# Optimization experiments

Measured on AMD Instinct MI355X. Metric: run time of the kernel, lower is better.

## Reference

```python
import jax, jax.numpy as jnp
import numpy as np

N_IN, N_OUT, F, H, E, V = 80, 25, 4096, 512, 512, 4096
B = 128
BOS = V - 3  # vocab = sorted words + ['<PAD>', '<BOS>', '<EOS>', '<UNK>']
LEAK = 0.01  # torch leaky_relu default slope


def gru_cell(x, h, wih, whh, bih, bhh):
    # PyTorch GRU gate order: [r, z, n]
    gi = x @ wih.T + bih
    gh = h @ whh.T + bhh
    ir, iz, inn = jnp.split(gi, 3, axis=-1)
    hr, hz, hn = jnp.split(gh, 3, axis=-1)
    r = jax.nn.sigmoid(ir + hr)
    z = jax.nn.sigmoid(iz + hz)
    n = jnp.tanh(inn + r * hn)
    return (1.0 - z) * n + z * h


def run_gru(xs, h0, wih, whh, bih, bhh):
    # xs: [T, B, D] -> outputs [T, B, H], final hidden [B, H]
    def step(h, x):
        h2 = gru_cell(x, h, wih, whh, bih, bhh)
        return h2, h2
    hT, ys = jax.lax.scan(step, h0, xs)
    return ys, hT


def setup_inputs() -> dict:
    key = jax.random.key(0)
    ks = jax.random.split(key, 10)

    def w(k, shape, fan_in):
        return jax.random.normal(k, shape, dtype=jnp.float32) / np.float32(np.sqrt(fan_in))

    return {
        "feats": jax.random.normal(ks[0], (N_IN, B, F), dtype=jnp.float32),
        "fc_w": w(ks[1], (E, F), F),
        "fc_b": jnp.zeros((E,), jnp.float32),
        "enc_wih": w(ks[2], (3 * H, E), E),
        "enc_whh": w(ks[3], (3 * H, H), H),
        "enc_bih": jnp.zeros((3 * H,), jnp.float32),
        "enc_bhh": jnp.zeros((3 * H,), jnp.float32),
        "dec_wih": w(ks[4], (3 * H, 2 * H + E), 2 * H + E),
        "dec_whh": w(ks[5], (3 * H, H), H),
        "dec_bih": jnp.zeros((3 * H,), jnp.float32),
        "dec_bhh": jnp.zeros((3 * H,), jnp.float32),
        "out_w": w(ks[6], (V, H), H),
        "out_b": jnp.zeros((V,), jnp.float32),
        "embed": jax.random.normal(ks[7], (V, E), dtype=jnp.float32) * 0.05,
        "tgt": jax.random.randint(ks[8], (B, N_OUT), 0, V, dtype=jnp.int32),
        "tfr": 0,
    }


def reference(feats, fc_w, fc_b, enc_wih, enc_whh, enc_bih, enc_bhh,
              dec_wih, dec_whh, dec_bih, dec_bhh, out_w, out_b, embed,
              tgt, tfr):
    T_in, Bv, _ = feats.shape
    # fc + leaky_relu (dropout = identity in eval)
    xp = jax.nn.leaky_relu(feats @ fc_w.T + fc_b, LEAK)            # [T_in, B, E]
    e_seq = jnp.concatenate([xp, jnp.zeros((N_OUT, Bv, E), xp.dtype)], axis=0)
    h0 = jnp.zeros((Bv, H), xp.dtype)
    enc_out, _ = run_gru(e_seq, h0, enc_wih, enc_whh, enc_bih, enc_bhh)  # [T_in+N_OUT, B, H]
    encA = jnp.transpose(enc_out[:T_in], (1, 0, 2))                # [B, T_in, H]
    # decoder pass 1 over encoding stage: input = [zeros(H+E) ; enc_out]
    dec1_in = jnp.concatenate(
        [jnp.zeros((T_in, Bv, H + E), xp.dtype), enc_out[:T_in]], axis=-1)
    _, alpha = run_gru(dec1_in, h0, dec_wih, dec_whh, dec_bih, dec_bhh)  # [B, H]

    d0 = jnp.broadcast_to(embed[BOS], (Bv, E))                     # <BOS> embedding
    enc_tail = enc_out[T_in:T_in + N_OUT]                          # [N_OUT, B, H]
    tgt_T = tgt.T                                                  # [N_OUT, B]

    def step(carry, inp):
        h, d = carry
        et_j, t_j = inp
        # dot-product attention over the T_in encoder states (Att_ linear is unused)
        s = jnp.tanh(jnp.einsum('bih,bh->bi', encA, h))            # [B, T_in]
        w = jax.nn.softmax(s, axis=1)
        c = jnp.einsum('bi,bih->bh', w, encA)                      # [B, H]
        x = jnp.concatenate([d, et_j, c], axis=-1)                 # [B, E+2H]
        h2 = gru_cell(x, h, dec_wih, dec_whh, dec_bih, dec_bhh)
        logp = jax.nn.log_softmax(h2 @ out_w.T + out_b, axis=-1)   # [B, V]
        lj = -jnp.mean(jnp.take_along_axis(logp, t_j[:, None], axis=1))
        d_next = embed[jnp.argmax(logp, axis=-1)]                  # greedy feedback (tfr=-1)
        return (h2, d_next), lj

    _, losses = jax.lax.scan(step, (alpha, d0), (enc_tail, tgt_T))
    return jnp.sum(losses) / N_OUT
```

## Files before the change

kernel.cpp:

```cpp
#include <hip/hip_runtime.h>
#include <hip/hip_bf16.h>

#define N_OUT 25
#define BOS   4093

typedef __attribute__((ext_vector_type(8))) short bf16x8;
typedef __attribute__((ext_vector_type(4))) float f32x4;

__device__ inline unsigned short f2bf(float f) {
    unsigned int u = __builtin_bit_cast(unsigned int, f);
    unsigned int r = (u + 0x7fffu + ((u >> 16) & 1u)) >> 16;
    return (unsigned short)r;
}
__device__ inline float bf2f(unsigned short s) {
    return __builtin_bit_cast(float, (unsigned int)s << 16);
}
__device__ inline float sigf(float x) { return 1.f / (1.f + expf(-x)); }

__device__ __forceinline__ unsigned long long ld_u64_coh(const void* p) {
    return __hip_atomic_load((const unsigned long long*)p, __ATOMIC_RELAXED, __HIP_MEMORY_SCOPE_AGENT);
}
__device__ __forceinline__ void st_u64_coh(void* p, unsigned long long v) {
    __hip_atomic_store((unsigned long long*)p, v, __ATOMIC_RELAXED, __HIP_MEMORY_SCOPE_AGENT);
}
__device__ __forceinline__ void st_u32_coh(void* p, unsigned int v) {
    __hip_atomic_store((unsigned int*)p, v, __ATOMIC_RELAXED, __HIP_MEMORY_SCOPE_AGENT);
}
__device__ __forceinline__ unsigned short ld_u16_coh(const unsigned short* p) {
    return __hip_atomic_load(p, __ATOMIC_RELAXED, __HIP_MEMORY_SCOPE_AGENT);
}
__device__ __forceinline__ int ld_i32_coh(const int* p) {
    return __hip_atomic_load(p, __ATOMIC_RELAXED, __HIP_MEMORY_SCOPE_AGENT);
}
__device__ __forceinline__ void st_i32_coh(int* p, int v) {
    __hip_atomic_store(p, v, __ATOMIC_RELAXED, __HIP_MEMORY_SCOPE_AGENT);
}
__device__ inline unsigned long long pack_ff(float a, float b) {
    return ((unsigned long long)__builtin_bit_cast(unsigned int, b) << 32) |
           __builtin_bit_cast(unsigned int, a);
}
__device__ inline unsigned long long pack_if(int a, float b) {
    return ((unsigned long long)__builtin_bit_cast(unsigned int, b) << 32) |
           (unsigned int)a;
}
__device__ __forceinline__ void spin_ge(const int* p, int tgt)
{
    while (ld_i32_coh(p) < tgt) __builtin_amdgcn_s_sleep(1);
}

__device__ __forceinline__ bf16x8 ld_bf8_sc1(const unsigned short* p) {
    bf16x8 r;
    asm volatile("global_load_dwordx4 %0, %1, off sc1" : "=v"(r) : "v"(p));
    return r;
}
#define VM_FENCE do { asm volatile("s_waitcnt vmcnt(0)" ::: "memory"); \
                      __builtin_amdgcn_sched_barrier(0); } while (0)

template<int AFP32, int OUT_BF, int ACT>
__global__ __launch_bounds__(256)
void gemm_mfma(const void* __restrict__ Ap, int lda,
               const unsigned short* __restrict__ W, int ldw,
               const float* __restrict__ bias,
               void* __restrict__ Cp, int ldc, int K)
{
    __shared__ short Abuf[128 * 32];
    __shared__ short Wbuf[128 * 32];
    const int tid  = threadIdx.x;
    const int lane = tid & 63;
    const int wave = tid >> 6;
    const int wr = wave >> 1, wc = wave & 1;
    const int l15 = lane & 15, kg = lane >> 4;
    const int m0 = blockIdx.y * 128, n0 = blockIdx.x * 128;

    const float* Af = (const float*)Ap;
    const unsigned short* Ab = (const unsigned short*)Ap;

    f32x4 acc[4][4];
#pragma unroll
    for (int i = 0; i < 4; ++i)
#pragma unroll
        for (int j = 0; j < 4; ++j) acc[i][j] = f32x4{0.f, 0.f, 0.f, 0.f};

    const bf16x8* Av = (const bf16x8*)Abuf;
    const bf16x8* Wv = (const bf16x8*)Wbuf;

    for (int k0 = 0; k0 < K; k0 += 32) {
#pragma unroll
        for (int cc = 0; cc < 2; ++cc) {
            int c = tid + cc * 256;
            int row = c >> 2, k8 = (c & 3) * 8;
            if (AFP32) {
                const float* src = &Af[(size_t)(m0 + row) * lda + k0 + k8];
                float4 v0 = *reinterpret_cast<const float4*>(src);
                float4 v1 = *reinterpret_cast<const float4*>(src + 4);
                bf16x8 s;
                s[0] = (short)f2bf(v0.x); s[1] = (short)f2bf(v0.y);
                s[2] = (short)f2bf(v0.z); s[3] = (short)f2bf(v0.w);
                s[4] = (short)f2bf(v1.x); s[5] = (short)f2bf(v1.y);
                s[6] = (short)f2bf(v1.z); s[7] = (short)f2bf(v1.w);
                *reinterpret_cast<bf16x8*>(&Abuf[row * 32 + k8]) = s;
            } else {
                *reinterpret_cast<bf16x8*>(&Abuf[row * 32 + k8]) =
                    *reinterpret_cast<const bf16x8*>(&Ab[(size_t)(m0 + row) * lda + k0 + k8]);
            }
            *reinterpret_cast<bf16x8*>(&Wbuf[row * 32 + k8]) =
                *reinterpret_cast<const bf16x8*>(&W[(size_t)(n0 + row) * ldw + k0 + k8]);
        }
        __syncthreads();
        bf16x8 a[4], b[4];
#pragma unroll
        for (int i = 0; i < 4; ++i) a[i] = Av[(wr * 64 + i * 16 + l15) * 4 + kg];
#pragma unroll
        for (int j = 0; j < 4; ++j) b[j] = Wv[(wc * 64 + j * 16 + l15) * 4 + kg];
#pragma unroll
        for (int i = 0; i < 4; ++i)
#pragma unroll
            for (int j = 0; j < 4; ++j)
                acc[i][j] = __builtin_amdgcn_mfma_f32_16x16x32_bf16(a[i], b[j], acc[i][j], 0, 0, 0);
        __syncthreads();
    }

    float* Cf = (float*)Cp;
    unsigned short* Cb = (unsigned short*)Cp;
#pragma unroll
    for (int i = 0; i < 4; ++i) {
#pragma unroll
        for (int j = 0; j < 4; ++j) {
            int n = n0 + wc * 64 + j * 16 + l15;
            float bv = bias[n];
#pragma unroll
            for (int r = 0; r < 4; ++r) {
                int m = m0 + wr * 64 + i * 16 + kg * 4 + r;
                float v = acc[i][j][r] + bv;
                if (ACT == 1) v = v > 0.f ? v : 0.01f * v;
                if (OUT_BF) Cb[(size_t)m * ldc + n] = f2bf(v);
                else        Cf[(size_t)m * ldc + n] = v;
            }
        }
    }
}

__global__ __launch_bounds__(256, 1)
void recur_persist(const unsigned short* __restrict__ enc_gi_bf,
                   const float* __restrict__ enc_bih, const float* __restrict__ enc_bhh,
                   const unsigned short* __restrict__ encwhh_bf,
                   const unsigned short* __restrict__ decwih_bf,
                   const unsigned short* __restrict__ decwhh_bf,
                   const float* __restrict__ dec_bih, const float* __restrict__ dec_bhh,
                   unsigned short* __restrict__ encout_bf,
                   unsigned short* __restrict__ hDb,
                   int* efl, int* dfl)
{
    __shared__ unsigned long long tileq[512];
    unsigned short* tile16 = (unsigned short*)tileq;
    const int g = blockIdx.x;
    const int tid = threadIdx.x, w = tid >> 6, lane = tid & 63;
    const int l15 = lane & 15, kg = lane >> 4;

    if (g < 32) {
        const int cg = g >> 1, rh = g & 1;
        const int mb = rh * 64 + w * 16;
        int wrow[6];
#pragma unroll
        for (int ct = 0; ct < 6; ++ct) wrow[ct] = (ct >> 1) * 512 + cg * 32 + (ct & 1) * 16 + l15;
        float hreg[2][4] = {{0.f,0.f,0.f,0.f},{0.f,0.f,0.f,0.f}};

        for (int i = 0; i < 105; ++i) {
            if (i > 0) {
                if (tid < 32) spin_ge(&efl[tid * 32], i);
                __syncthreads();
                asm volatile("" ::: "memory");
            }
            bf16x8 areg[16];
            if (i > 0) {
                const unsigned short* ap = &encout_bf[(size_t)(i - 1) * 65536 + (size_t)(mb + l15) * 512 + kg * 8];
                VM_FENCE;
#pragma unroll
                for (int ks = 0; ks < 16; ++ks) areg[ks] = ld_bf8_sc1(ap + ks * 32);
                VM_FENCE;
            } else {
#pragma unroll
                for (int ks = 0; ks < 16; ++ks) areg[ks] = bf16x8{0,0,0,0,0,0,0,0};
            }
            f32x4 acc[6];
#pragma unroll
            for (int ct = 0; ct < 6; ++ct) acc[ct] = f32x4{0.f, 0.f, 0.f, 0.f};
#pragma unroll
            for (int ks = 0; ks < 16; ++ks) {
#pragma unroll
                for (int ct = 0; ct < 6; ++ct) {
                    bf16x8 bv = *(const bf16x8*)&encwhh_bf[(size_t)wrow[ct] * 512 + ks * 32 + kg * 8];
                    acc[ct] = __builtin_amdgcn_mfma_f32_16x16x32_bf16(areg[ks], bv, acc[ct], 0, 0, 0);
                }
            }
#pragma unroll
            for (int jh = 0; jh < 2; ++jh) {
                int jc = cg * 32 + jh * 16 + l15;
                float bhr = enc_bhh[jc], bhz = enc_bhh[512 + jc], bhn = enc_bhh[1024 + jc];
#pragma unroll
                for (int rr = 0; rr < 4; ++rr) {
                    int br = mb + kg * 4 + rr;
                    float gr_, gz_, gn_;
                    if (i < 80) {
                        const unsigned short* gp = enc_gi_bf + ((size_t)i * 128 + br) * 1536 + jc;
                        gr_ = bf2f(gp[0]); gz_ = bf2f(gp[512]); gn_ = bf2f(gp[1024]);
                    } else {
                        gr_ = enc_bih[jc]; gz_ = enc_bih[512 + jc]; gn_ = enc_bih[1024 + jc];
                    }
                    float r = sigf(gr_ + bhr + acc[jh][rr]);
                    float z = sigf(gz_ + bhz + acc[2 + jh][rr]);
                    float n = tanhf(gn_ + r * (acc[4 + jh][rr] + bhn));
                    float v = (1.f - z) * n + z * hreg[jh][rr];
                    hreg[jh][rr] = v;
                    tile16[(w * 16 + kg * 4 + rr) * 32 + jh * 16 + l15] = f2bf(v);
                }
            }
            __syncthreads();
            {
                size_t base = (size_t)i * 65536 + (size_t)(rh * 64) * 512 + cg * 32;
                int row = tid >> 3, ch = tid & 7;
                st_u64_coh(&encout_bf[base + (size_t)row * 512 + ch * 4], tileq[tid]);
                st_u64_coh(&encout_bf[base + (size_t)(32 + row) * 512 + ch * 4], tileq[256 + tid]);
            }
            __syncthreads();
            if (tid == 0) st_i32_coh(&efl[g * 32], i + 1);
        }
    } else {
        const int s = g - 32;
        const int cg = s >> 2, rq = s & 3;
        const int rt = w >> 1, cs = w & 1;
        const int mb = rq * 32 + rt * 16;
        int wrow[3];
#pragma unroll
        for (int t = 0; t < 3; ++t) wrow[t] = t * 512 + cg * 32 + cs * 16 + l15;
        const int jc = cg * 32 + cs * 16 + l15;
        float hreg[4] = {0.f, 0.f, 0.f, 0.f};

        for (int i = 1; i <= 80; ++i) {
            if (tid < 32) spin_ge(&efl[tid * 32], i);
            else if (tid >= 64 && tid < 128 && i >= 2) spin_ge(&dfl[(tid - 64) * 32], i - 1);
            __syncthreads();
            asm volatile("" ::: "memory");

            f32x4 agi[3], agh[3];
#pragma unroll
            for (int t = 0; t < 3; ++t) { agi[t] = f32x4{0.f,0.f,0.f,0.f}; agh[t] = f32x4{0.f,0.f,0.f,0.f}; }
            bf16x8 areg[16];
            {
                const unsigned short* ap = &encout_bf[(size_t)(i - 1) * 65536 + (size_t)(mb + l15) * 512 + kg * 8];
                VM_FENCE;
#pragma unroll
                for (int ks = 0; ks < 16; ++ks) areg[ks] = ld_bf8_sc1(ap + ks * 32);
                VM_FENCE;
            }
#pragma unroll
            for (int ks = 0; ks < 16; ++ks)
#pragma unroll
                for (int t = 0; t < 3; ++t) {
                    bf16x8 bv = *(const bf16x8*)&decwih_bf[(size_t)wrow[t] * 1536 + 1024 + ks * 32 + kg * 8];
                    agi[t] = __builtin_amdgcn_mfma_f32_16x16x32_bf16(areg[ks], bv, agi[t], 0, 0, 0);
                }
            if (i >= 2) {
                const unsigned short* ap = &hDb[(size_t)((i - 1) & 1) * 65536 + (size_t)(mb + l15) * 512 + kg * 8];
                VM_FENCE;
#pragma unroll
                for (int ks = 0; ks < 16; ++ks) areg[ks] = ld_bf8_sc1(ap + ks * 32);
                VM_FENCE;
            } else {
#pragma unroll
                for (int ks = 0; ks < 16; ++ks) areg[ks] = bf16x8{0,0,0,0,0,0,0,0};
            }
#pragma unroll
            for (int ks = 0; ks < 16; ++ks)
#pragma unroll
                for (int t = 0; t < 3; ++t) {
                    bf16x8 bv = *(const bf16x8*)&decwhh_bf[(size_t)wrow[t] * 512 + ks * 32 + kg * 8];
                    agh[t] = __builtin_amdgcn_mfma_f32_16x16x32_bf16(areg[ks], bv, agh[t], 0, 0, 0);
                }
            float bir = dec_bih[jc], bhr = dec_bhh[jc];
            float biz = dec_bih[512 + jc], bhz = dec_bhh[512 + jc];
            float bin_ = dec_bih[1024 + jc], bhn = dec_bhh[1024 + jc];
#pragma unroll
            for (int rr = 0; rr < 4; ++rr) {
                float r = sigf(agi[0][rr] + bir + agh[0][rr] + bhr);
                float z = sigf(agi[1][rr] + biz + agh[1][rr] + bhz);
                float n = tanhf(agi[2][rr] + bin_ + r * (agh[2][rr] + bhn));
                float v = (1.f - z) * n + z * hreg[rr];
                hreg[rr] = v;
                tile16[(rt * 16 + kg * 4 + rr) * 32 + cs * 16 + l15] = f2bf(v);
            }
            __syncthreads();
            {
                size_t base = (size_t)(i & 1) * 65536 + (size_t)(rq * 32) * 512 + cg * 32;
                int row = tid >> 3, ch = tid & 7;
                st_u64_coh(&hDb[base + (size_t)row * 512 + ch * 4], tileq[tid]);
            }
            __syncthreads();
            if (tid == 0) st_i32_coh(&dfl[s * 32], i);
        }
    }
}

__device__ void attention(int b, const unsigned short* __restrict__ hrow,
                          unsigned short* __restrict__ c_bf,
                          float* hsh, float* ssh, const unsigned short* esh)
{
    const int tid = threadIdx.x;
    if (tid < 128) {
        unsigned long long u = ld_u64_coh(&hrow[tid * 4]);
        hsh[tid * 4 + 0] = bf2f((unsigned short)(u));
        hsh[tid * 4 + 1] = bf2f((unsigned short)(u >> 16));
        hsh[tid * 4 + 2] = bf2f((unsigned short)(u >> 32));
        hsh[tid * 4 + 3] = bf2f((unsigned short)(u >> 48));
    }
    __syncthreads();
    const int wv = tid >> 6, lane = tid & 63;
    float hreg[8];
#pragma unroll
    for (int q = 0; q < 8; ++q) hreg[q] = hsh[lane * 8 + q];
#pragma unroll 4
    for (int i = wv; i < 80; i += 4) {
        bf16x8 v = *(const bf16x8*)&esh[i * 512 + lane * 8];
        float p = 0.f;
#pragma unroll
        for (int q = 0; q < 8; ++q) p += bf2f((unsigned short)v[q]) * hreg[q];
#pragma unroll
        for (int off = 32; off > 0; off >>= 1) p += __shfl_xor(p, off, 64);
        if (lane == 0) ssh[i] = tanhf(p);
    }
    __syncthreads();
    if (tid == 0) {
        float mx = -1e30f;
        for (int i = 0; i < 80; ++i) mx = fmaxf(mx, ssh[i]);
        float s = 0.f;
        for (int i = 0; i < 80; ++i) { float e = expf(ssh[i] - mx); ssh[i] = e; s += e; }
        ssh[80] = 1.0f / s;
    }
    __syncthreads();
    float acc0 = 0.f, acc1 = 0.f;
    const unsigned short* ebase = esh + tid * 2;
#pragma unroll 10
    for (int i = 0; i < 80; ++i) {
        unsigned int u = *reinterpret_cast<const unsigned int*>(&ebase[i * 512]);
        float w = ssh[i];
        acc0 += w * __builtin_bit_cast(float, u << 16);
        acc1 += w * __builtin_bit_cast(float, u & 0xffff0000u);
    }
    float inv = ssh[80];
    unsigned int packed = (unsigned int)f2bf(acc0 * inv) | ((unsigned int)f2bf(acc1 * inv) << 16);
    st_u32_coh(&c_bf[(size_t)b * 512 + tid * 2], packed);
    __syncthreads();
}

__global__ __launch_bounds__(256, 1)
void decode_persist(const unsigned short* __restrict__ encout_bf,
                    const unsigned short* __restrict__ decwih_bf, const unsigned short* __restrict__ decwhh_bf,
                    const float* __restrict__ dec_bhh,
                    const unsigned short* __restrict__ outw_bf, const float* __restrict__ out_b,
                    const unsigned short* __restrict__ emb2gi, const float* __restrict__ gie,
                    const int* __restrict__ tgt,
                    const unsigned short* __restrict__ hDb,
                    unsigned short* __restrict__ hCb,
                    unsigned short* __restrict__ c_bf,
                    unsigned long long* __restrict__ pA, unsigned long long* __restrict__ pB,
                    float* __restrict__ out,
                    int* c1, int* cp, int* c2)
{
    __shared__ unsigned short esh[80 * 512];
    __shared__ float hsh[512];
    __shared__ float ssh[88];
    __shared__ unsigned long long tileq[256];
    __shared__ float sMv[256];
    __shared__ int   sIv[256];
    __shared__ float sLv[256];
    __shared__ int   sVid[32];
    unsigned short* tile16 = (unsigned short*)tileq;

    const int g = blockIdx.x;
    const int tid = threadIdx.x, w = tid >> 6, lane = tid & 63;
    const int l15 = lane & 15, kg = lane >> 4;
    float loss_acc = 0.f;

    for (int i = w; i < 80; i += 4)
        *(bf16x8*)&esh[i * 512 + lane * 8] =
            *(const bf16x8*)&encout_bf[(size_t)i * 65536 + g * 512 + lane * 8];
    __syncthreads();

    attention(g, hDb + (size_t)g * 512, c_bf, hsh, ssh, esh);
    __syncthreads();
    if (tid == 0) st_i32_coh(&c2[g * 32], 1);

    const int cg = g >> 2, rq = g & 3;
    const int rt = w >> 1, cs = w & 1;
    const int mb = rq * 32 + rt * 16;
    const int jc = cg * 32 + cs * 16 + l15;
    int wrow[3];
#pragma unroll
    for (int t = 0; t < 3; ++t) wrow[t] = t * 512 + cg * 32 + cs * 16 + l15;
    float hreg[4] = {0.f, 0.f, 0.f, 0.f};
    if (g < 64) {
#pragma unroll
        for (int rr = 0; rr < 4; ++rr)
            hreg[rr] = bf2f(ld_u16_coh(&hDb[(size_t)(mb + kg * 4 + rr) * 512 + jc]));
    }

    for (int j = 0; j < 25; ++j) {
        unsigned short* h_out_b = hCb + (size_t)(j & 1) * 65536;
        unsigned long long* pAj = pA + (size_t)(j & 1) * 16384;
        unsigned long long* pBj = pB + (size_t)(j & 1) * 16384;
        const unsigned long long* pAp = pA + (size_t)((j - 1) & 1) * 16384;
        const unsigned long long* pBp = pB + (size_t)((j - 1) & 1) * 16384;

        if (g < 64) {
            const unsigned short* h_in_b = (j == 0) ? hDb : hCb + (size_t)((j - 1) & 1) * 65536;
            if (tid < 128) spin_ge(&c2[tid * 32], j + 1);
            __syncthreads();
            asm volatile("" ::: "memory");

            f32x4 agi[3], agh[3];
#pragma unroll
            for (int t = 0; t < 3; ++t) { agi[t] = f32x4{0.f,0.f,0.f,0.f}; agh[t] = f32x4{0.f,0.f,0.f,0.f}; }
            bf16x8 areg[16];

            {
                const unsigned short* ap = &c_bf[(size_t)(mb + l15) * 512 + kg * 8];
                VM_FENCE;
#pragma unroll
                for (int ks = 0; ks < 16; ++ks) areg[ks] = ld_bf8_sc1(ap + ks * 32);
                VM_FENCE;
            }
#pragma unroll
            for (int ks = 0; ks < 16; ++ks)
#pragma unroll
                for (int t = 0; t < 3; ++t) {
                    bf16x8 bv = *(const bf16x8*)&decwih_bf[(size_t)wrow[t] * 1536 + 1024 + ks * 32 + kg * 8];
                    agi[t] = __builtin_amdgcn_mfma_f32_16x16x32_bf16(areg[ks], bv, agi[t], 0, 0, 0);
                }
            {
                const unsigned short* ap = &h_in_b[(size_t)(mb + l15) * 512 + kg * 8];
                VM_FENCE;
#pragma unroll
                for (int ks = 0; ks < 16; ++ks) areg[ks] = ld_bf8_sc1(ap + ks * 32);
                VM_FENCE;
            }
#pragma unroll
            for (int ks = 0; ks < 16; ++ks)
#pragma unroll
                for (int t = 0; t < 3; ++t) {
                    bf16x8 bv = *(const bf16x8*)&decwhh_bf[(size_t)wrow[t] * 512 + ks * 32 + kg * 8];
                    agh[t] = __builtin_amdgcn_mfma_f32_16x16x32_bf16(areg[ks], bv, agh[t], 0, 0, 0);
                }

            int myvid[4];
            if (j == 0) {
#pragma unroll
                for (int rr = 0; rr < 4; ++rr) myvid[rr] = BOS;
            } else {
                if (tid < 128) spin_ge(&cp[tid * 32], j);
                __syncthreads();
                asm volatile("" ::: "memory");
                const int rowl = tid >> 3, seg = tid & 7;
                const int browg = rq * 32 + rowl;
                float bm = -1e30f; int bi = 0x7fffffff;
#pragma unroll
                for (int half = 0; half < 2; ++half) {
                    unsigned long long ua[8], ub[8];
#pragma unroll
                    for (int k = 0; k < 8; ++k)
                        ua[k] = ld_u64_coh(&pAp[(size_t)browg * 128 + seg * 16 + half * 8 + k]);
#pragma unroll
                    for (int k = 0; k < 8; ++k)
                        ub[k] = ld_u64_coh(&pBp[(size_t)browg * 128 + seg * 16 + half * 8 + k]);
#pragma unroll
                    for (int k = 0; k < 8; ++k) {
                        float m = __builtin_bit_cast(float, (unsigned int)ua[k]);
                        int ii = (int)(unsigned int)ub[k];
                        if (m > bm || (m == bm && ii < bi)) { bm = m; bi = ii; }
                    }
                }
                sMv[tid] = bm; sIv[tid] = bi;
                __syncthreads();
                if (seg == 0) {
                    float m = sMv[tid]; int ii = sIv[tid];
#pragma unroll
                    for (int k = 1; k < 8; ++k) {
                        float om = sMv[tid + k]; int oi = sIv[tid + k];
                        if (om > m || (om == m && oi < ii)) { m = om; ii = oi; }
                    }
                    sVid[rowl] = ii;
                }
                __syncthreads();
#pragma unroll
                for (int rr = 0; rr < 4; ++rr) myvid[rr] = sVid[rt * 16 + kg * 4 + rr];
            }

            float bhr = dec_bhh[jc], bhz = dec_bhh[512 + jc], bhn = dec_bhh[1024 + jc];
#pragma unroll
            for (int rr = 0; rr < 4; ++rr) {
                int br = mb + kg * 4 + rr;
                const float* gp = &gie[((size_t)j * 128 + br) * 1536 + jc];
                const unsigned short* ep = &emb2gi[(size_t)myvid[rr] * 1536 + jc];
                float g0 = gp[0]    + bf2f(ep[0]);
                float g1 = gp[512]  + bf2f(ep[512]);
                float g2 = gp[1024] + bf2f(ep[1024]);
                float r = sigf(g0 + agi[0][rr] + agh[0][rr] + bhr);
                float z = sigf(g1 + agi[1][rr] + agh[1][rr] + bhz);
                float n = tanhf(g2 + agi[2][rr] + r * (agh[2][rr] + bhn));
                float v = (1.f - z) * n + z * hreg[rr];
                hreg[rr] = v;
                tile16[(rt * 16 + kg * 4 + rr) * 32 + cs * 16 + l15] = f2bf(v);
            }
            __syncthreads();
            {
                size_t base = (size_t)(j & 1) * 65536 + (size_t)(rq * 32) * 512 + cg * 32;
                int row = tid >> 3, ch = tid & 7;
                st_u64_coh(&hCb[base + (size_t)row * 512 + ch * 4], tileq[tid]);
            }
            __syncthreads();
            if (tid == 0) st_i32_coh(&c1[g * 32], j + 1);
        }

        {
            if (tid < 64) spin_ge(&c1[tid * 32], j + 1);
            __syncthreads();
            asm volatile("" ::: "memory");

            if (j < 24) attention(g, h_out_b + (size_t)g * 512, c_bf, hsh, ssh, esh);
            __syncthreads();
            if (tid == 0) st_i32_coh(&c2[g * 32], j + 2);

            const int n0 = g * 32;
            f32x4 acc[2][2];
#pragma unroll
            for (int mt = 0; mt < 2; ++mt)
#pragma unroll
                for (int nt = 0; nt < 2; ++nt) acc[mt][nt] = f32x4{0.f,0.f,0.f,0.f};
            bf16x8 ar0[16], ar1[16];
            {
                const unsigned short* p0 = &h_out_b[(size_t)(w * 32 + l15) * 512 + kg * 8];
                const unsigned short* p1 = &h_out_b[(size_t)(w * 32 + 16 + l15) * 512 + kg * 8];
                VM_FENCE;
#pragma unroll
                for (int ks = 0; ks < 16; ++ks) ar0[ks] = ld_bf8_sc1(p0 + ks * 32);
#pragma unroll
                for (int ks = 0; ks < 16; ++ks) ar1[ks] = ld_bf8_sc1(p1 + ks * 32);
                VM_FENCE;
            }
#pragma unroll
            for (int ks = 0; ks < 16; ++ks) {
                bf16x8 b0 = *(const bf16x8*)&outw_bf[(size_t)(n0 + l15) * 512 + ks * 32 + kg * 8];
                bf16x8 b1 = *(const bf16x8*)&outw_bf[(size_t)(n0 + 16 + l15) * 512 + ks * 32 + kg * 8];
                acc[0][0] = __builtin_amdgcn_mfma_f32_16x16x32_bf16(ar0[ks], b0, acc[0][0], 0, 0, 0);
                acc[0][1] = __builtin_amdgcn_mfma_f32_16x16x32_bf16(ar0[ks], b1, acc[0][1], 0, 0, 0);
                acc[1][0] = __builtin_amdgcn_mfma_f32_16x16x32_bf16(ar1[ks], b0, acc[1][0], 0, 0, 0);
                acc[1][1] = __builtin_amdgcn_mfma_f32_16x16x32_bf16(ar1[ks], b1, acc[1][1], 0, 0, 0);
            }
            float ob0 = out_b[n0 + l15], ob1 = out_b[n0 + 16 + l15];
#pragma unroll
            for (int mt = 0; mt < 2; ++mt) {
#pragma unroll
                for (int rr = 0; rr < 4; ++rr) {
                    int m = w * 32 + mt * 16 + kg * 4 + rr;
                    float v0 = acc[mt][0][rr] + ob0;
                    float v1 = acc[mt][1][rr] + ob1;
                    int tj = tgt[m * 25 + j];
                    float pm; int pi;
                    if (v0 >= v1) { pm = v0; pi = n0 + l15; }
                    else          { pm = v1; pi = n0 + 16 + l15; }
                    float pl = -1e30f;
                    if (n0 + l15 == tj)      pl = v0;
                    if (n0 + 16 + l15 == tj) pl = v1;
#pragma unroll
                    for (int off = 1; off < 16; off <<= 1) {
                        float om = __shfl_xor(pm, off, 64);
                        int   oi = __shfl_xor(pi, off, 64);
                        float ol = __shfl_xor(pl, off, 64);
                        if (om > pm || (om == pm && oi < pi)) { pm = om; pi = oi; }
                        pl = fmaxf(pl, ol);
                    }
                    float ps = expf(v0 - pm) + expf(v1 - pm);
#pragma unroll
                    for (int off = 1; off < 16; off <<= 1) ps += __shfl_xor(ps, off, 64);
                    if (l15 == 0) {
                        st_u64_coh(&pAj[(size_t)m * 128 + g], pack_ff(pm, ps));
                        st_u64_coh(&pBj[(size_t)m * 128 + g], pack_if(pi, pl));
                    }
                }
            }
            __syncthreads();
            if (tid == 0) st_i32_coh(&cp[g * 32], j + 1);
        }

        if (g >= 64) {
            if (tid < 128) spin_ge(&cp[tid * 32], j + 1);
            __syncthreads();
            asm volatile("" ::: "memory");
            const int rowb = (g - 64) * 2 + (tid >> 7);
            const int t2 = tid & 127;
            unsigned long long ua = ld_u64_coh(&pAj[(size_t)rowb * 128 + t2]);
            unsigned long long ub = ld_u64_coh(&pBj[(size_t)rowb * 128 + t2]);
            float m_ = __builtin_bit_cast(float, (unsigned int)ua);
            float s_ = __builtin_bit_cast(float, (unsigned int)(ua >> 32));
            float l_ = __builtin_bit_cast(float, (unsigned int)(ub >> 32));
            sMv[tid] = m_; sLv[tid] = l_;
            __syncthreads();
            for (int st = 64; st > 0; st >>= 1) {
                if (t2 < st) {
                    sMv[tid] = fmaxf(sMv[tid], sMv[tid + st]);
                    sLv[tid] = fmaxf(sLv[tid], sLv[tid + st]);
                }
                __syncthreads();
            }
            float M = sMv[tid & 128];
            float LT = sLv[tid & 128];
            __syncthreads();
            sMv[tid] = s_ * expf(m_ - M);
            __syncthreads();
            for (int st = 64; st > 0; st >>= 1) {
                if (t2 < st) sMv[tid] += sMv[tid + st];
                __syncthreads();
            }
            if (t2 == 0) loss_acc += -(LT - (M + logf(sMv[tid])));
            __syncthreads();
        }
    }

    if (g >= 64 && (tid == 0 || tid == 128))
        atomicAdd(out, loss_acc * (1.0f / 3200.0f));
}

__global__ __launch_bounds__(256)
void cast_all(const float* __restrict__ fc_w, const float* __restrict__ enc_wih,
              const float* __restrict__ enc_whh, const float* __restrict__ dec_wih,
              const float* __restrict__ dec_whh, const float* __restrict__ out_w,
              const float* __restrict__ embed,
              unsigned short* __restrict__ d_fcw, unsigned short* __restrict__ d_encwih,
              unsigned short* __restrict__ d_encwhh, unsigned short* __restrict__ d_decwih,
              unsigned short* __restrict__ d_decwhh, unsigned short* __restrict__ d_outw,
              unsigned short* __restrict__ d_embed)
{
    long i = (long)(blockIdx.x * 256 + threadIdx.x) * 4;
    const float* s; unsigned short* d; long off;
    if      (i <  2097152) { s = fc_w;    d = d_fcw;    off = 0; }
    else if (i <  2883584) { s = enc_wih; d = d_encwih; off = 2097152; }
    else if (i <  3670016) { s = enc_whh; d = d_encwhh; off = 2883584; }
    else if (i <  6029312) { s = dec_wih; d = d_decwih; off = 3670016; }
    else if (i <  6815744) { s = dec_whh; d = d_decwhh; off = 6029312; }
    else if (i <  8912896) { s = out_w;   d = d_outw;   off = 6815744; }
    else if (i < 11010048) { s = embed;   d = d_embed;  off = 8912896; }
    else return;
    i -= off;
    float4 v = *reinterpret_cast<const float4*>(&s[i]);
    d[i + 0] = f2bf(v.x); d[i + 1] = f2bf(v.y);
    d[i + 2] = f2bf(v.z); d[i + 3] = f2bf(v.w);
}

extern "C" void kernel_launch(void* const* d_in, const int* in_sizes, int n_in,
                              void* d_out, int out_size, void* d_ws, size_t ws_size,
                              hipStream_t stream)
{
    const float* feats   = (const float*)d_in[0];
    const float* fc_w    = (const float*)d_in[1];
    const float* fc_b    = (const float*)d_in[2];
    const float* enc_wih = (const float*)d_in[3];
    const float* enc_whh = (const float*)d_in[4];
    const float* enc_bih = (const float*)d_in[5];
    const float* enc_bhh = (const float*)d_in[6];
    const float* dec_wih = (const float*)d_in[7];
    const float* dec_whh = (const float*)d_in[8];
    const float* dec_bih = (const float*)d_in[9];
    const float* dec_bhh = (const float*)d_in[10];
    const float* out_w   = (const float*)d_in[11];
    const float* out_b   = (const float*)d_in[12];
    const float* embed   = (const float*)d_in[13];
    const int*   tgt     = (const int*)d_in[14];

    float* ws = (float*)d_ws;
    size_t off = 0;
    auto afl = [&](size_t n) { float* r = ws + off; off += n; return r; };

    unsigned short* enc_gi_bf = (unsigned short*)afl(7864320);
    unsigned short* encout_bf = (unsigned short*)afl(3440640);
    unsigned short* xp_bf     = (unsigned short*)afl(2621440);
    unsigned short* fcw_bf    = (unsigned short*)afl(1048576);
    unsigned short* encwih_bf = (unsigned short*)afl(393216);
    unsigned short* encwhh_bf = (unsigned short*)afl(393216);
    unsigned short* decwih_bf = (unsigned short*)afl(1179648);
    unsigned short* decwhh_bf = (unsigned short*)afl(393216);
    unsigned short* outw_bf   = (unsigned short*)afl(1048576);
    unsigned short* embed_bf  = (unsigned short*)afl(1048576);
    unsigned short* emb2gi    = (unsigned short*)afl(3145728);
    float* gie               = afl(4915200);
    float* zbias             = afl(1536);
    unsigned short* hDb       = (unsigned short*)afl(65536);
    unsigned short* hCb       = (unsigned short*)afl(65536);
    unsigned short* c_bf      = (unsigned short*)afl(32768);
    unsigned long long* pA   = (unsigned long long*)afl(65536);
    unsigned long long* pB   = (unsigned long long*)afl(65536);
    int* flags               = (int*)afl(16384);

    int* efl = flags;
    int* dfl = flags + 32 * 32;
    int* c1  = flags + 96 * 32;
    int* cp  = flags + 160 * 32;
    int* c2  = flags + 288 * 32;

    hipMemsetAsync(zbias, 0, 1536 * sizeof(float), stream);
    hipMemsetAsync(flags, 0, 16384 * sizeof(int), stream);
    hipMemsetAsync(d_out, 0, sizeof(float), stream);

    cast_all<<<10752, 256, 0, stream>>>(fc_w, enc_wih, enc_whh, dec_wih, dec_whh, out_w, embed,
                                        fcw_bf, encwih_bf, encwhh_bf, decwih_bf, decwhh_bf,
                                        outw_bf, embed_bf);

    gemm_mfma<1, 1, 1><<<dim3(4, 80), 256, 0, stream>>>(feats, 4096, fcw_bf, 4096, fc_b, xp_bf, 512, 4096);
    gemm_mfma<0, 1, 0><<<dim3(12, 80), 256, 0, stream>>>(xp_bf, 512, encwih_bf, 512, enc_bih, enc_gi_bf, 1536, 512);
    gemm_mfma<0, 1, 0><<<dim3(12, 32), 256, 0, stream>>>(embed_bf, 512, decwih_bf, 1536, zbias, emb2gi, 1536, 512);

    recur_persist<<<96, 256, 0, stream>>>(enc_gi_bf, enc_bih, enc_bhh, encwhh_bf,
                                          decwih_bf, decwhh_bf, dec_bih, dec_bhh,
                                          encout_bf, hDb, efl, dfl);

    gemm_mfma<0, 0, 0><<<dim3(12, 25), 256, 0, stream>>>(encout_bf + (size_t)80 * 65536, 512,
                                                         decwih_bf + 512, 1536, dec_bih, gie, 1536, 512);

    decode_persist<<<128, 256, 0, stream>>>(encout_bf, decwih_bf, decwhh_bf,
                                            dec_bhh, outw_bf, out_b,
                                            emb2gi, gie, tgt,
                                            hDb, hCb, c_bf, pA, pB, (float*)d_out,
                                            c1, cp, c2);
}
```

Before: 3.385 ms.

## Split encoder GRU by batch rows to remove cross-block step barriers

Each encoder block now owns 16 batch rows across all 512 hidden columns, keeping its hidden state in shared memory, so the 105 sequential steps no longer need a grid-wide flag barrier among 32 blocks. The block count drops to 8, each doing 4x more MFMA work per step and reading the full recurrent weight matrix every step. The decoder-side blocks now poll only 8 flags, and the two A-operand loads are issued together before the MFMA loops to overlap their latency. The trade is less parallelism and more weight traffic per block in exchange for removing inter-block synchronization latency on the critical path.

```diff
diff --git a/kernel.cpp b/kernel.cpp
--- a/kernel.cpp
+++ b/kernel.cpp
@@ -151,55 +151,61 @@
                    unsigned short* __restrict__ hDb,
                    int* efl, int* dfl)
 {
+    __shared__ unsigned short h_tile[16 * 528];
     __shared__ unsigned long long tileq[512];
     unsigned short* tile16 = (unsigned short*)tileq;
+
     const int g = blockIdx.x;
     const int tid = threadIdx.x, w = tid >> 6, lane = tid & 63;
     const int l15 = lane & 15, kg = lane >> 4;
 
-    if (g < 32) {
-        const int cg = g >> 1, rh = g & 1;
-        const int mb = rh * 64 + w * 16;
-        int wrow[6];
-#pragma unroll
-        for (int ct = 0; ct < 6; ++ct) wrow[ct] = (ct >> 1) * 512 + cg * 32 + (ct & 1) * 16 + l15;
-        float hreg[2][4] = {{0.f,0.f,0.f,0.f},{0.f,0.f,0.f,0.f}};
+    if (g < 8) {
+        const int R0 = g * 16;
+        const int wc0 = w * 128;
+        for (int idx = tid; idx < 16 * 528; idx += 256) h_tile[idx] = 0;
+        float hp[8][4];
+#pragma unroll
+        for (int c8 = 0; c8 < 8; ++c8)
+#pragma unroll
+            for (int rr = 0; rr < 4; ++rr) hp[c8][rr] = 0.f;
+        __syncthreads();
 
         for (int i = 0; i < 105; ++i) {
-            if (i > 0) {
-                if (tid < 32) spin_ge(&efl[tid * 32], i);
-                __syncthreads();
-                asm volatile("" ::: "memory");
-            }
-            bf16x8 areg[16];
-            if (i > 0) {
-                const unsigned short* ap = &encout_bf[(size_t)(i - 1) * 65536 + (size_t)(mb + l15) * 512 + kg * 8];
-                VM_FENCE;
-#pragma unroll
-                for (int ks = 0; ks < 16; ++ks) areg[ks] = ld_bf8_sc1(ap + ks * 32);
-                VM_FENCE;
-            } else {
-#pragma unroll
-                for (int ks = 0; ks < 16; ++ks) areg[ks] = bf16x8{0,0,0,0,0,0,0,0};
-            }
-            f32x4 acc[6];
-#pragma unroll
-            for (int ct = 0; ct < 6; ++ct) acc[ct] = f32x4{0.f, 0.f, 0.f, 0.f};
-#pragma unroll
-            for (int ks = 0; ks < 16; ++ks) {
-#pragma unroll
-                for (int ct = 0; ct < 6; ++ct) {
-                    bf16x8 bv = *(const bf16x8*)&encwhh_bf[(size_t)wrow[ct] * 512 + ks * 32 + kg * 8];
-                    acc[ct] = __builtin_amdgcn_mfma_f32_16x16x32_bf16(areg[ks], bv, acc[ct], 0, 0, 0);
-                }
-            }
-#pragma unroll
-            for (int jh = 0; jh < 2; ++jh) {
-                int jc = cg * 32 + jh * 16 + l15;
+            bf16x8 a[16];
+#pragma unroll
+            for (int ks = 0; ks < 16; ++ks)
+                a[ks] = *(const bf16x8*)&h_tile[l15 * 528 + ks * 32 + kg * 8];
+            __syncthreads();
+
+            f32x4 acc[3][8];
+#pragma unroll
+            for (int t = 0; t < 3; ++t)
+#pragma unroll
+                for (int c8 = 0; c8 < 8; ++c8) acc[t][c8] = f32x4{0.f,0.f,0.f,0.f};
+#pragma unroll
+            for (int t = 0; t < 3; ++t) {
+#pragma unroll
+                for (int c8 = 0; c8 < 8; ++c8) {
+                    const unsigned short* bp =
+                        encwhh_bf + (size_t)(t * 512 + wc0 + c8 * 16 + l15) * 512 + kg * 8;
+#pragma unroll
+                    for (int ks = 0; ks < 16; ++ks) {
+                        bf16x8 bv = *(const bf16x8*)&bp[ks * 32];
+                        acc[t][c8] = __builtin_amdgcn_mfma_f32_16x16x32_bf16(a[ks], bv, acc[t][c8], 0, 0, 0);
+                    }
+                }
+            }
+
+            if (i > 0 && tid == 0) st_i32_coh(&efl[g * 32], i);
+
+#pragma unroll
+            for (int c8 = 0; c8 < 8; ++c8) {
+                int jc = wc0 + c8 * 16 + l15;
                 float bhr = enc_bhh[jc], bhz = enc_bhh[512 + jc], bhn = enc_bhh[1024 + jc];
 #pragma unroll
                 for (int rr = 0; rr < 4; ++rr) {
-                    int br = mb + kg * 4 + rr;
+                    int row = kg * 4 + rr;
+                    int br = R0 + row;
                     float gr_, gz_, gn_;
                     if (i < 80) {
                         const unsigned short* gp = enc_gi_bf + ((size_t)i * 128 + br) * 1536 + jc;
@@ -207,26 +213,30 @@
                     } else {
                         gr_ = enc_bih[jc]; gz_ = enc_bih[512 + jc]; gn_ = enc_bih[1024 + jc];
                     }
-                    float r = sigf(gr_ + bhr + acc[jh][rr]);
-                    float z = sigf(gz_ + bhz + acc[2 + jh][rr]);
-                    float n = tanhf(gn_ + r * (acc[4 + jh][rr] + bhn));
-                    float v = (1.f - z) * n + z * hreg[jh][rr];
-                    hreg[jh][rr] = v;
-                    tile16[(w * 16 + kg * 4 + rr) * 32 + jh * 16 + l15] = f2bf(v);
-                }
-            }
-            __syncthreads();
+                    float r = sigf(gr_ + bhr + acc[0][c8][rr]);
+                    float z = sigf(gz_ + bhz + acc[1][c8][rr]);
+                    float n = tanhf(gn_ + r * (acc[2][c8][rr] + bhn));
+                    float v = (1.f - z) * n + z * hp[c8][rr];
+                    hp[c8][rr] = v;
+                    h_tile[row * 528 + jc] = f2bf(v);
+                }
+            }
+            __syncthreads();
+
             {
-                size_t base = (size_t)i * 65536 + (size_t)(rh * 64) * 512 + cg * 32;
-                int row = tid >> 3, ch = tid & 7;
-                st_u64_coh(&encout_bf[base + (size_t)row * 512 + ch * 4], tileq[tid]);
-                st_u64_coh(&encout_bf[base + (size_t)(32 + row) * 512 + ch * 4], tileq[256 + tid]);
-            }
-            __syncthreads();
-            if (tid == 0) st_i32_coh(&efl[g * 32], i + 1);
+                int row = tid >> 4, part = tid & 15;
+                const unsigned long long* src = (const unsigned long long*)&h_tile[row * 528 + part * 32];
+                unsigned long long* dst = (unsigned long long*)
+                    &encout_bf[(size_t)i * 65536 + (size_t)(R0 + row) * 512 + part * 32];
+#pragma unroll
+                for (int k = 0; k < 8; ++k) st_u64_coh(&dst[k], src[k]);
+            }
         }
+        VM_FENCE;
+        __syncthreads();
+        if (tid == 0) st_i32_coh(&efl[g * 32], 105);
     } else {
-        const int s = g - 32;
+        const int s = g - 8;
         const int cg = s >> 2, rq = s & 3;
         const int rt = w >> 1, cs = w & 1;
         const int mb = rq * 32 + rt * 16;
@@ -237,45 +247,45 @@
         float hreg[4] = {0.f, 0.f, 0.f, 0.f};
 
         for (int i = 1; i <= 80; ++i) {
-            if (tid < 32) spin_ge(&efl[tid * 32], i);
+            if (tid < 8) spin_ge(&efl[tid * 32], i);
             else if (tid >= 64 && tid < 128 && i >= 2) spin_ge(&dfl[(tid - 64) * 32], i - 1);
             __syncthreads();
             asm volatile("" ::: "memory");
 
+            bf16x8 a1[16], a2[16];
+            {
+                const unsigned short* p1 = &encout_bf[(size_t)(i - 1) * 65536 + (size_t)(mb + l15) * 512 + kg * 8];
+                VM_FENCE;
+#pragma unroll
+                for (int ks = 0; ks < 16; ++ks) a1[ks] = ld_bf8_sc1(p1 + ks * 32);
+                if (i >= 2) {
+                    const unsigned short* p2 = &hDb[(size_t)((i - 1) & 1) * 65536 + (size_t)(mb + l15) * 512 + kg * 8];
+#pragma unroll
+                    for (int ks = 0; ks < 16; ++ks) a2[ks] = ld_bf8_sc1(p2 + ks * 32);
+                }
+                VM_FENCE;
+            }
+            if (i < 2) {
+#pragma unroll
+                for (int ks = 0; ks < 16; ++ks) a2[ks] = bf16x8{0,0,0,0,0,0,0,0};
+            }
+
             f32x4 agi[3], agh[3];
 #pragma unroll
             for (int t = 0; t < 3; ++t) { agi[t] = f32x4{0.f,0.f,0.f,0.f}; agh[t] = f32x4{0.f,0.f,0.f,0.f}; }
-            bf16x8 areg[16];
-            {
-                const unsigned short* ap = &encout_bf[(size_t)(i - 1) * 65536 + (size_t)(mb + l15) * 512 + kg * 8];
-                VM_FENCE;
-#pragma unroll
-                for (int ks = 0; ks < 16; ++ks) areg[ks] = ld_bf8_sc1(ap + ks * 32);
-                VM_FENCE;
-            }
 #pragma unroll
             for (int ks = 0; ks < 16; ++ks)
 #pragma unroll
                 for (int t = 0; t < 3; ++t) {
                     bf16x8 bv = *(const bf16x8*)&decwih_bf[(size_t)wrow[t] * 1536 + 1024 + ks * 32 + kg * 8];
-                    agi[t] = __builtin_amdgcn_mfma_f32_16x16x32_bf16(areg[ks], bv, agi[t], 0, 0, 0);
-                }
-            if (i >= 2) {
-                const unsigned short* ap = &hDb[(size_t)((i - 1) & 1) * 65536 + (size_t)(mb + l15) * 512 + kg * 8];
-                VM_FENCE;
-#pragma unroll
-                for (int ks = 0; ks < 16; ++ks) areg[ks] = ld_bf8_sc1(ap + ks * 32);
-                VM_FENCE;
-            } else {
-#pragma unroll
-                for (int ks = 0; ks < 16; ++ks) areg[ks] = bf16x8{0,0,0,0,0,0,0,0};
-            }
+                    agi[t] = __builtin_amdgcn_mfma_f32_16x16x32_bf16(a1[ks], bv, agi[t], 0, 0, 0);
+                }
 #pragma unroll
             for (int ks = 0; ks < 16; ++ks)
 #pragma unroll
                 for (int t = 0; t < 3; ++t) {
                     bf16x8 bv = *(const bf16x8*)&decwhh_bf[(size_t)wrow[t] * 512 + ks * 32 + kg * 8];
-                    agh[t] = __builtin_amdgcn_mfma_f32_16x16x32_bf16(areg[ks], bv, agh[t], 0, 0, 0);
+                    agh[t] = __builtin_amdgcn_mfma_f32_16x16x32_bf16(a2[ks], bv, agh[t], 0, 0, 0);
                 }
             float bir = dec_bih[jc], bhr = dec_bhh[jc];
             float biz = dec_bih[512 + jc], bhz = dec_bhh[512 + jc];
@@ -420,13 +430,15 @@
             f32x4 agi[3], agh[3];
 #pragma unroll
             for (int t = 0; t < 3; ++t) { agi[t] = f32x4{0.f,0.f,0.f,0.f}; agh[t] = f32x4{0.f,0.f,0.f,0.f}; }
-            bf16x8 areg[16];
-
+            bf16x8 aC[16], aH[16];
             {
-                const unsigned short* ap = &c_bf[(size_t)(mb + l15) * 512 + kg * 8];
+                const unsigned short* pc = &c_bf[(size_t)(mb + l15) * 512 + kg * 8];
+                const unsigned short* ph = &h_in_b[(size_t)(mb + l15) * 512 + kg * 8];
                 VM_FENCE;
 #pragma unroll
-                for (int ks = 0; ks < 16; ++ks) areg[ks] = ld_bf8_sc1(ap + ks * 32);
+                for (int ks = 0; ks < 16; ++ks) aC[ks] = ld_bf8_sc1(pc + ks * 32);
+#pragma unroll
+                for (int ks = 0; ks < 16; ++ks) aH[ks] = ld_bf8_sc1(ph + ks * 32);
                 VM_FENCE;
             }
 #pragma unroll
@@ -434,21 +446,14 @@
 #pragma unroll
                 for (int t = 0; t < 3; ++t) {
                     bf16x8 bv = *(const bf16x8*)&decwih_bf[(size_t)wrow[t] * 1536 + 1024 + ks * 32 + kg * 8];
-                    agi[t] = __builtin_amdgcn_mfma_f32_16x16x32_bf16(areg[ks], bv, agi[t], 0, 0, 0);
-                }
-            {
-                const unsigned short* ap = &h_in_b[(size_t)(mb + l15) * 512 + kg * 8];
-                VM_FENCE;
-#pragma unroll
-                for (int ks = 0; ks < 16; ++ks) areg[ks] = ld_bf8_sc1(ap + ks * 32);
-                VM_FENCE;
-            }
+                    agi[t] = __builtin_amdgcn_mfma_f32_16x16x32_bf16(aC[ks], bv, agi[t], 0, 0, 0);
+                }
 #pragma unroll
             for (int ks = 0; ks < 16; ++ks)
 #pragma unroll
                 for (int t = 0; t < 3; ++t) {
                     bf16x8 bv = *(const bf16x8*)&decwhh_bf[(size_t)wrow[t] * 512 + ks * 32 + kg * 8];
-                    agh[t] = __builtin_amdgcn_mfma_f32_16x16x32_bf16(areg[ks], bv, agh[t], 0, 0, 0);
+                    agh[t] = __builtin_amdgcn_mfma_f32_16x16x32_bf16(aH[ks], bv, agh[t], 0, 0, 0);
                 }
 
             int myvid[4];
@@ -717,7 +722,7 @@
     gemm_mfma<0, 1, 0><<<dim3(12, 80), 256, 0, stream>>>(xp_bf, 512, encwih_bf, 512, enc_bih, enc_gi_bf, 1536, 512);
     gemm_mfma<0, 1, 0><<<dim3(12, 32), 256, 0, stream>>>(embed_bf, 512, decwih_bf, 1536, zbias, emb2gi, 1536, 512);
 
-    recur_persist<<<96, 256, 0, stream>>>(enc_gi_bf, enc_bih, enc_bhh, encwhh_bf,
+    recur_persist<<<72, 256, 0, stream>>>(enc_gi_bf, enc_bih, enc_bhh, encwhh_bf,
                                           decwih_bf, decwhh_bf, dec_bih, dec_bhh,
                                           encout_bf, hDb, efl, dfl);
 
```

Result: slower. 7.580 ms (+123.9%).
